# Kernel tuning notes

Hardware: AMD Instinct MI355X
Metric: run time of the kernel (lower is better)

## Reference

```python
import jax, jax.numpy as jnp
import numpy as np

N = 50000   # nodes
E = 600000  # edges
IN = 128    # in_channels
H = 128     # hidden
G = 64      # graphs in batch


def setup_inputs() -> dict:
    key = jax.random.key(0)
    ks = jax.random.split(key, 12)
    x = jax.random.normal(ks[0], (N, IN), jnp.float32)
    edge_index = jax.random.randint(ks[1], (2, E), 0, N, dtype=jnp.int64)
    batch = jnp.sort(jax.random.randint(ks[2], (N,), 0, G, dtype=jnp.int64))

    def glorot(k, i, o):
        return jax.random.normal(k, (i, o), jnp.float32) / np.float32(np.sqrt(i))

    return {
        "x": x, "edge_index": edge_index, "batch": batch,
        "W1": glorot(ks[3], IN, H), "b1": jnp.zeros((H,), jnp.float32),
        "W2": glorot(ks[4], H, H),  "b2": jnp.zeros((H,), jnp.float32),
        "W3": glorot(ks[5], H, H),  "b3": jnp.zeros((H,), jnp.float32),
        "Wl": glorot(ks[6], H, 2),  "bl": jnp.zeros((2,), jnp.float32),
    }


def gcn_conv(x, W, b, src, dst, n):
    # PyG GCNConv: linear transform, add self-loops, symmetric deg^-1/2 norm, scatter-add.
    h = x @ W                                   # [n, H]
    loop = jnp.arange(n, dtype=src.dtype)
    s = jnp.concatenate([src, loop])            # [E+n]
    d = jnp.concatenate([dst, loop])
    deg = jax.ops.segment_sum(jnp.ones_like(d, jnp.float32), d, num_segments=n)
    dinv = jax.lax.rsqrt(deg)                   # deg >= 1 thanks to self-loops
    norm = dinv[s] * dinv[d]                    # [E+n]
    out = jax.ops.segment_sum(h[s] * norm[:, None], d, num_segments=n)
    return out + b


def reference(x, edge_index, batch, W1, b1, W2, b2, W3, b3, Wl, bl):
    src, dst = edge_index[0], edge_index[1]
    h = jax.nn.relu(gcn_conv(x, W1, b1, src, dst, N))
    h = jax.nn.relu(gcn_conv(h, W2, b2, src, dst, N))
    h = jax.nn.relu(gcn_conv(h, W3, b3, src, dst, N))
    # global_mean_pool over graph ids
    cnt = jax.ops.segment_sum(jnp.ones((N,), jnp.float32), batch, num_segments=G)
    pooled = jax.ops.segment_sum(h, batch, num_segments=G) / jnp.maximum(cnt, 1.0)[:, None]
    # dropout is identity in eval mode
    return pooled @ Wl + bl                     # [G, 2]
```

## Files before the change

### kernel.cpp

```cpp
#include <hip/hip_runtime.h>


#define THREADS 256
#define ELLW 48
#define ELLS 64
#define BCAP 4096
#define EPB  4096

typedef __attribute__((ext_vector_type(8))) short short8;
typedef __attribute__((ext_vector_type(4))) float f32x4;
typedef __attribute__((ext_vector_type(2))) float floatx2;

__device__ inline void bf16_split(float f, unsigned short& hi, unsigned short& lo) {
    unsigned u = __float_as_uint(f);
    unsigned r = u + 0x7FFF + ((u >> 16) & 1);
    hi = (unsigned short)(r >> 16);
    float hf = __uint_as_float((unsigned)hi << 16);
    float lf = f - hf;
    unsigned ul = __float_as_uint(lf);
    lo = (unsigned short)((ul + 0x7FFF + ((ul >> 16) & 1)) >> 16);
}
__device__ inline unsigned pack_bf16(float a, float b) {
    unsigned ua = __float_as_uint(a);
    unsigned ub = __float_as_uint(b);
    ua += 0x7FFF + ((ua >> 16) & 1);
    ub += 0x7FFF + ((ub >> 16) & 1);
    return (ua >> 16) | (ub & 0xFFFF0000u);
}
__device__ inline floatx2 fp8x2_to_f32(unsigned short u) {
    return __builtin_amdgcn_cvt_pk_f32_fp8((int)(unsigned)u, false);
}
__device__ inline unsigned char f32_to_fp8(float v) {
    int pk = __builtin_amdgcn_cvt_pk_fp8_f32(v, v, 0, false);
    return (unsigned char)(pk & 0xFF);
}

__global__ __launch_bounds__(THREADS) void prep_k(const float* __restrict__ W1,
                                                  const float* __restrict__ W2,
                                                  const float* __restrict__ W3,
                                                  unsigned* __restrict__ wf,
                                                  const int* __restrict__ batch,
                                                  int* __restrict__ gstart,
                                                  int* __restrict__ gcur,
                                                  int n, int gtot, int nb) {
    int b = blockIdx.x;
    if (b < 3) {
        const float* W = (b == 0) ? W1 : (b == 1) ? W2 : W3;
        unsigned* o_hi = wf + (size_t)b * 16384;
        unsigned* o_lo = o_hi + 8192;
        for (int o = threadIdx.x; o < 8192; o += THREADS) {
            int d = o & 3, l = (o >> 2) & 63, ts = o >> 8;
            int s = ts & 3, t = ts >> 2;
            int k = s * 32 + ((l >> 4) << 3) + d * 2;
            int nn = t * 16 + (l & 15);
            float v0 = W[k * 128 + nn];
            float v1 = W[(k + 1) * 128 + nn];
            unsigned short h0, l0, h1, l1;
            bf16_split(v0, h0, l0);
            bf16_split(v1, h1, l1);
            o_hi[o] = (unsigned)h0 | ((unsigned)h1 << 16);
            o_lo[o] = (unsigned)l0 | ((unsigned)l1 << 16);
        }
    } else if (b == 3) {
        int t = threadIdx.x;
        if (t <= gtot) {
            int lo = 0, hi = n;
            while (lo < hi) {
                int mid = (lo + hi) >> 1;
                if (batch[mid] < t) lo = mid + 1; else hi = mid;
            }
            gstart[t] = lo;
        }
    } else {
        int t = threadIdx.x;
        if (t < nb) gcur[t] = 0;
    }
}

__global__ __launch_bounds__(THREADS) void part1_k(const int* __restrict__ src,
                                                   const int* __restrict__ dst,
                                                   int* __restrict__ gcur,
                                                   unsigned* __restrict__ region,
                                                   int e, int nb) {
    __shared__ int hist[256];
    __shared__ int base[256];
    int tid = threadIdx.x;
    hist[tid] = 0;
    __syncthreads();
    int start = blockIdx.x * EPB;
#pragma unroll
    for (int j = 0; j < EPB / THREADS; ++j) {
        int i = start + j * THREADS + tid;
        if (i < e) atomicAdd(&hist[dst[i] >> 8], 1);
    }
    __syncthreads();
    if (tid < nb) base[tid] = atomicAdd(&gcur[tid], hist[tid]);
    hist[tid] = 0;
    __syncthreads();
#pragma unroll
    for (int j = 0; j < EPB / THREADS; ++j) {
        int i = start + j * THREADS + tid;
        if (i < e) {
            int d = dst[i], s = src[i];
            int bk = d >> 8;
            int lp = atomicAdd(&hist[bk], 1);
            int pos = base[bk] + lp;
            if (pos < BCAP)
                region[(size_t)bk * BCAP + pos] = ((unsigned)(d & 255) << 16) | (unsigned)s;
        }
    }
}

__global__ __launch_bounds__(THREADS) void part2_k(const unsigned* __restrict__ region,
                                                   const int* __restrict__ gcur,
                                                   int* __restrict__ ell, int n) {
    __shared__ int cnt[256];
    int tid = threadIdx.x;
    int b = blockIdx.x;
    cnt[tid] = 0;
    __syncthreads();
    int nbk = min(gcur[b], BCAP);
    for (int i = tid; i < nbk; i += THREADS) {
        unsigned u = region[(size_t)b * BCAP + i];
        int dloc = (int)(u >> 16);
        int pos = atomicAdd(&cnt[dloc], 1);
        if (pos < ELLW)
            ell[(size_t)(b * 256 + dloc) * ELLS + 1 + pos] = (int)(u & 0xFFFFu);
    }
    __syncthreads();
    int node = b * 256 + tid;
    if (node < n) ell[(size_t)node * ELLS] = cnt[tid];
}

template <bool ABF16>
__global__ __launch_bounds__(THREADS) void mfma_gemm_k(const void* __restrict__ Av,
                                                       const unsigned* __restrict__ wf,
                                                       const int* __restrict__ ell,
                                                       unsigned char* __restrict__ g8,
                                                       int n) {
    __shared__ unsigned wls[16384];
    int tid = threadIdx.x;
    int lane = tid & 63;
    int r0 = blockIdx.x * 64 + (tid >> 6) * 16;

    for (int i = tid; i < 4096; i += THREADS)
        ((uint4*)wls)[i] = ((const uint4*)wf)[i];

    f32x4 acc[8];
#pragma unroll
    for (int t = 0; t < 8; ++t) acc[t] = (f32x4){0.f, 0.f, 0.f, 0.f};

    int arow = min(r0 + (lane & 15), n - 1);
    int kcol = (lane >> 4) << 3;

    short8 ah[4], al[4];
    if (ABF16) {
        const unsigned short* A = (const unsigned short*)Av;
#pragma unroll
        for (int s = 0; s < 4; ++s)
            ah[s] = *(const short8*)&A[(size_t)arow * 128 + kcol + s * 32];
    } else {
        const float* A = (const float*)Av;
        float4 v0[4], v1[4];
#pragma unroll
        for (int s = 0; s < 4; ++s) {
            v0[s] = *(const float4*)&A[(size_t)arow * 128 + kcol + s * 32];
            v1[s] = *(const float4*)&A[(size_t)arow * 128 + kcol + s * 32 + 4];
        }
#pragma unroll
        for (int s = 0; s < 4; ++s) {
            unsigned short h[8], lo[8];
            bf16_split(v0[s].x, h[0], lo[0]); bf16_split(v0[s].y, h[1], lo[1]);
            bf16_split(v0[s].z, h[2], lo[2]); bf16_split(v0[s].w, h[3], lo[3]);
            bf16_split(v1[s].x, h[4], lo[4]); bf16_split(v1[s].y, h[5], lo[5]);
            bf16_split(v1[s].z, h[6], lo[6]); bf16_split(v1[s].w, h[7], lo[7]);
#pragma unroll
            for (int j = 0; j < 8; ++j) { ah[s][j] = (short)h[j]; al[s][j] = (short)lo[j]; }
        }
    }

    __syncthreads();

#pragma unroll
    for (int s = 0; s < 4; ++s) {
#pragma unroll
        for (int t = 0; t < 8; ++t) {
            int base = (t * 4 + s) * 256 + lane * 4;
            short8 bh = *(short8*)&wls[base];
            short8 bl = *(short8*)&wls[8192 + base];
            acc[t] = __builtin_amdgcn_mfma_f32_16x16x32_bf16(ah[s], bh, acc[t], 0, 0, 0);
            if (!ABF16)
                acc[t] = __builtin_amdgcn_mfma_f32_16x16x32_bf16(al[s], bh, acc[t], 0, 0, 0);
            acc[t] = __builtin_amdgcn_mfma_f32_16x16x32_bf16(ah[s], bl, acc[t], 0, 0, 0);
        }
    }

    int rbase = r0 + ((lane >> 4) << 2);
#pragma unroll
    for (int reg = 0; reg < 4; ++reg) {
        int rr = rbase + reg;
        if (rr < n) {
            float dv = rsqrtf(1.f + (float)ell[(size_t)rr * ELLS]);
#pragma unroll
            for (int t = 0; t < 8; ++t)
                g8[(size_t)rr * 128 + t * 16 + (lane & 15)] = f32_to_fp8(acc[t][reg] * dv);
        }
    }
}

__global__ __launch_bounds__(THREADS) void aggregate_k(const unsigned short* __restrict__ g8u,
                                                       const int* __restrict__ ell,
                                                       const float* __restrict__ bias,
                                                       unsigned* __restrict__ h16,
                                                       int n) {
    int wave = (blockIdx.x * THREADS + threadIdx.x) >> 6;
    int lane = threadIdx.x & 63;
    if (wave >= n) return;

    int v = ell[(size_t)wave * ELLS + lane];
    int cnt_true = __shfl(v, 0);
    int deg = min(cnt_true, ELLW);

    floatx2 fs = fp8x2_to_f32(g8u[(size_t)wave * 64 + lane]);
    float ax0 = fs.x, ay0 = fs.y;
    float ax1 = 0.f, ay1 = 0.f, ax2 = 0.f, ay2 = 0.f, ax3 = 0.f, ay3 = 0.f;
    float ax4 = 0.f, ay4 = 0.f, ax5 = 0.f, ay5 = 0.f, ax6 = 0.f, ay6 = 0.f;
    float ax7 = 0.f, ay7 = 0.f;

    for (int k = 0; k < deg; k += 8) {
        int s0 = __shfl(v, k + 1);
        int s1 = __shfl(v, min(k + 2, deg));
        int s2 = __shfl(v, min(k + 3, deg));
        int s3 = __shfl(v, min(k + 4, deg));
        int s4 = __shfl(v, min(k + 5, deg));
        int s5 = __shfl(v, min(k + 6, deg));
        int s6 = __shfl(v, min(k + 7, deg));
        int s7 = __shfl(v, min(k + 8, deg));
        float m1 = (k + 1 < deg) ? 1.f : 0.f;
        float m2 = (k + 2 < deg) ? 1.f : 0.f;
        float m3 = (k + 3 < deg) ? 1.f : 0.f;
        float m4 = (k + 4 < deg) ? 1.f : 0.f;
        float m5 = (k + 5 < deg) ? 1.f : 0.f;
        float m6 = (k + 6 < deg) ? 1.f : 0.f;
        float m7 = (k + 7 < deg) ? 1.f : 0.f;
        unsigned short q0 = g8u[(size_t)s0 * 64 + lane];
        unsigned short q1 = g8u[(size_t)s1 * 64 + lane];
        unsigned short q2 = g8u[(size_t)s2 * 64 + lane];
        unsigned short q3 = g8u[(size_t)s3 * 64 + lane];
        unsigned short q4 = g8u[(size_t)s4 * 64 + lane];
        unsigned short q5 = g8u[(size_t)s5 * 64 + lane];
        unsigned short q6 = g8u[(size_t)s6 * 64 + lane];
        unsigned short q7 = g8u[(size_t)s7 * 64 + lane];
        floatx2 f0 = fp8x2_to_f32(q0);
        floatx2 f1 = fp8x2_to_f32(q1);
        floatx2 f2 = fp8x2_to_f32(q2);
        floatx2 f3 = fp8x2_to_f32(q3);
        floatx2 f4 = fp8x2_to_f32(q4);
        floatx2 f5 = fp8x2_to_f32(q5);
        floatx2 f6 = fp8x2_to_f32(q6);
        floatx2 f7 = fp8x2_to_f32(q7);
        ax0 += f0.x;                ay0 += f0.y;
        ax1 = fmaf(m1, f1.x, ax1);  ay1 = fmaf(m1, f1.y, ay1);
        ax2 = fmaf(m2, f2.x, ax2);  ay2 = fmaf(m2, f2.y, ay2);
        ax3 = fmaf(m3, f3.x, ax3);  ay3 = fmaf(m3, f3.y, ay3);
        ax4 = fmaf(m4, f4.x, ax4);  ay4 = fmaf(m4, f4.y, ay4);
        ax5 = fmaf(m5, f5.x, ax5);  ay5 = fmaf(m5, f5.y, ay5);
        ax6 = fmaf(m6, f6.x, ax6);  ay6 = fmaf(m6, f6.y, ay6);
        ax7 = fmaf(m7, f7.x, ax7);  ay7 = fmaf(m7, f7.y, ay7);
    }
    ax0 += (ax1 + ax2) + (ax3 + ax4) + (ax5 + ax6) + ax7;
    ay0 += (ay1 + ay2) + (ay3 + ay4) + (ay5 + ay6) + ay7;

    float d = rsqrtf(1.f + (float)cnt_true);
    float2 bb = ((const float2*)bias)[lane];
    float ox = fmaxf(fmaf(d, ax0, bb.x), 0.f);
    float oy = fmaxf(fmaf(d, ay0, bb.y), 0.f);
    h16[(size_t)wave * 64 + lane] = pack_bf16(ox, oy);
}

#define PSLICES 8
__global__ __launch_bounds__(THREADS) void pool_k(const unsigned* __restrict__ h16,
                                                  const int* __restrict__ gstart,
                                                  float* __restrict__ partial) {
    int gph = blockIdx.x, s = blockIdx.y;
    int start = gstart[gph], end = gstart[gph + 1];
    int len = end - start;
    int chunk = (len + PSLICES - 1) / PSLICES;
    int rs = start + s * chunk;
    int re = min(rs + chunk, end);
    int c = threadIdx.x & 63, half = threadIdx.x >> 6;
    float sx = 0.f, sy = 0.f;
    for (int r = rs + half; r < re; r += 4) {
        unsigned u = h16[(size_t)r * 64 + c];
        sx += __uint_as_float(u << 16);
        sy += __uint_as_float(u & 0xFFFF0000u);
    }
    __shared__ float shx[4][64], shy[4][64];
    shx[half][c] = sx;
    shy[half][c] = sy;
    __syncthreads();
    if (half == 0) {
        sx = shx[0][c] + shx[1][c] + shx[2][c] + shx[3][c];
        sy = shy[0][c] + shy[1][c] + shy[2][c] + shy[3][c];
        partial[(gph * PSLICES + s) * 128 + c * 2] = sx;
        partial[(gph * PSLICES + s) * 128 + c * 2 + 1] = sy;
    }
}

__global__ __launch_bounds__(128) void final_k(const float* __restrict__ partial,
                                               const int* __restrict__ gstart,
                                               const float* __restrict__ Wl,
                                               const float* __restrict__ bl,
                                               float* __restrict__ out, int gtot) {
    int t = threadIdx.x;
    int gph = t >> 1, j = t & 1;
    if (gph >= gtot) return;
    float cnt = fmaxf((float)(gstart[gph + 1] - gstart[gph]), 1.f);
    float sacc = 0.f;
    for (int k = 0; k < 128; ++k) {
        float v = 0.f;
#pragma unroll
        for (int sb = 0; sb < PSLICES; ++sb)
            v += partial[(gph * PSLICES + sb) * 128 + k];
        sacc = fmaf(v, Wl[k * 2 + j], sacc);
    }
    out[gph * 2 + j] = sacc / cnt + bl[j];
}

extern "C" void kernel_launch(void* const* d_in, const int* in_sizes, int n_in,
                              void* d_out, int out_size, void* d_ws, size_t ws_size,
                              hipStream_t stream) {
    const float* x  = (const float*)d_in[0];
    const int* ei   = (const int*)d_in[1];
    const int* batch= (const int*)d_in[2];
    const float* W1 = (const float*)d_in[3];
    const float* b1 = (const float*)d_in[4];
    const float* W2 = (const float*)d_in[5];
    const float* b2 = (const float*)d_in[6];
    const float* W3 = (const float*)d_in[7];
    const float* b3 = (const float*)d_in[8];
    const float* Wl = (const float*)d_in[9];
    const float* bl = (const float*)d_in[10];
    float* out = (float*)d_out;

    const int N = in_sizes[0] / 128;
    const int E = in_sizes[1] / 2;
    const int G = out_size / 2;
    const int* src = ei;
    const int* dst = ei + E;
    const int NB = (N + 255) >> 8;

    char* ws = (char*)d_ws;
    size_t off = 0;
    auto alloc = [&](size_t bytes) -> void* {
        void* p = ws + off;
        off = (off + bytes + 255) & ~(size_t)255;
        return p;
    };
    unsigned char* g8 = (unsigned char*)alloc((size_t)N * 128);
    unsigned* h16   = (unsigned*)alloc((size_t)N * 64 * 4);
    int* ell        = (int*)alloc((size_t)N * ELLS * 4);
    unsigned* wf    = (unsigned*)alloc((size_t)3 * 16384 * 4);
    unsigned* region= (unsigned*)alloc((size_t)NB * BCAP * 4);
    int* gcur       = (int*)alloc((size_t)NB * 4);
    float* partial  = (float*)alloc((size_t)G * PSLICES * 128 * 4);
    int* gstart     = (int*)alloc((size_t)(G + 1) * 4);
    (void)ws_size;

    int grid1 = (E + EPB - 1) / EPB;
    int gemmGrid = (N + 63) / 64;
    int aggGrid = (N + 3) / 4;
    unsigned short* g8u = (unsigned short*)g8;

    prep_k<<<5, THREADS, 0, stream>>>(W1, W2, W3, wf, batch, gstart, gcur, N, G, NB);
    part1_k<<<grid1, THREADS, 0, stream>>>(src, dst, gcur, region, E, NB);
    part2_k<<<NB, THREADS, 0, stream>>>(region, gcur, ell, N);

    mfma_gemm_k<false><<<gemmGrid, THREADS, 0, stream>>>(x, wf, ell, g8, N);
    aggregate_k<<<aggGrid, THREADS, 0, stream>>>(g8u, ell, b1, h16, N);
    mfma_gemm_k<true><<<gemmGrid, THREADS, 0, stream>>>(h16, wf + 16384, ell, g8, N);
    aggregate_k<<<aggGrid, THREADS, 0, stream>>>(g8u, ell, b2, h16, N);
    mfma_gemm_k<true><<<gemmGrid, THREADS, 0, stream>>>(h16, wf + 32768, ell, g8, N);
    aggregate_k<<<aggGrid, THREADS, 0, stream>>>(g8u, ell, b3, h16, N);

    dim3 poolGrid(G, PSLICES);
    pool_k<<<poolGrid, THREADS, 0, stream>>>(h16, gstart, partial);
    final_k<<<1, 128, 0, stream>>>(partial, gstart, Wl, bl, out, G);
}
```

Measured before the change: 174.9 us.

## Pack ELL neighbor indices as 16-bit and unroll aggregation to 16 gathers

The ELL adjacency now stores neighbor indices as 16-bit values, two per dword, with the count in the first dword. This halves the row stride to 32 ints while raising capacity to 62 neighbors. The aggregation kernel unpacks indices via shuffles and issues 16 independent gathers per iteration, with masking on loaded values, to raise memory-level parallelism. It relies on source node ids fitting in 16 bits, which fails for N=50000 beyond 65535. The base already truncated to 16 bits via the region packing.

```diff
diff --git a/kernel.cpp b/kernel.cpp
--- a/kernel.cpp
+++ b/kernel.cpp
@@ -2,8 +2,8 @@
 
 
 #define THREADS 256
-#define ELLW 48
-#define ELLS 64
+#define ELLW 62
+#define ELLD 32
 #define BCAP 4096
 #define EPB  4096
 
@@ -119,17 +119,18 @@
     int b = blockIdx.x;
     cnt[tid] = 0;
     __syncthreads();
+    unsigned short* ell16 = (unsigned short*)ell;
     int nbk = min(gcur[b], BCAP);
     for (int i = tid; i < nbk; i += THREADS) {
         unsigned u = region[(size_t)b * BCAP + i];
         int dloc = (int)(u >> 16);
         int pos = atomicAdd(&cnt[dloc], 1);
         if (pos < ELLW)
-            ell[(size_t)(b * 256 + dloc) * ELLS + 1 + pos] = (int)(u & 0xFFFFu);
+            ell16[(size_t)(b * 256 + dloc) * (ELLD * 2) + 2 + pos] = (unsigned short)(u & 0xFFFFu);
     }
     __syncthreads();
     int node = b * 256 + tid;
-    if (node < n) ell[(size_t)node * ELLS] = cnt[tid];
+    if (node < n) ell[(size_t)node * ELLD] = cnt[tid];
 }
 
 template <bool ABF16>
@@ -200,7 +201,7 @@
     for (int reg = 0; reg < 4; ++reg) {
         int rr = rbase + reg;
         if (rr < n) {
-            float dv = rsqrtf(1.f + (float)ell[(size_t)rr * ELLS]);
+            float dv = rsqrtf(1.f + (float)ell[(size_t)rr * ELLD]);
 #pragma unroll
             for (int t = 0; t < 8; ++t)
                 g8[(size_t)rr * 128 + t * 16 + (lane & 15)] = f32_to_fp8(acc[t][reg] * dv);
@@ -209,7 +210,7 @@
 }
 
 __global__ __launch_bounds__(THREADS) void aggregate_k(const unsigned short* __restrict__ g8u,
-                                                       const int* __restrict__ ell,
+                                                       const unsigned* __restrict__ ell,
                                                        const float* __restrict__ bias,
                                                        unsigned* __restrict__ h16,
                                                        int n) {
@@ -217,64 +218,45 @@
     int lane = threadIdx.x & 63;
     if (wave >= n) return;
 
-    int v = ell[(size_t)wave * ELLS + lane];
-    int cnt_true = __shfl(v, 0);
+    unsigned v = ell[(size_t)wave * ELLD + (lane & 31)];
+    int cnt_true = (int)__shfl((int)v, 0);
     int deg = min(cnt_true, ELLW);
+    int dm1 = max(deg - 1, 0);
 
     floatx2 fs = fp8x2_to_f32(g8u[(size_t)wave * 64 + lane]);
-    float ax0 = fs.x, ay0 = fs.y;
-    float ax1 = 0.f, ay1 = 0.f, ax2 = 0.f, ay2 = 0.f, ax3 = 0.f, ay3 = 0.f;
-    float ax4 = 0.f, ay4 = 0.f, ax5 = 0.f, ay5 = 0.f, ax6 = 0.f, ay6 = 0.f;
-    float ax7 = 0.f, ay7 = 0.f;
-
-    for (int k = 0; k < deg; k += 8) {
-        int s0 = __shfl(v, k + 1);
-        int s1 = __shfl(v, min(k + 2, deg));
-        int s2 = __shfl(v, min(k + 3, deg));
-        int s3 = __shfl(v, min(k + 4, deg));
-        int s4 = __shfl(v, min(k + 5, deg));
-        int s5 = __shfl(v, min(k + 6, deg));
-        int s6 = __shfl(v, min(k + 7, deg));
-        int s7 = __shfl(v, min(k + 8, deg));
-        float m1 = (k + 1 < deg) ? 1.f : 0.f;
-        float m2 = (k + 2 < deg) ? 1.f : 0.f;
-        float m3 = (k + 3 < deg) ? 1.f : 0.f;
-        float m4 = (k + 4 < deg) ? 1.f : 0.f;
-        float m5 = (k + 5 < deg) ? 1.f : 0.f;
-        float m6 = (k + 6 < deg) ? 1.f : 0.f;
-        float m7 = (k + 7 < deg) ? 1.f : 0.f;
-        unsigned short q0 = g8u[(size_t)s0 * 64 + lane];
-        unsigned short q1 = g8u[(size_t)s1 * 64 + lane];
-        unsigned short q2 = g8u[(size_t)s2 * 64 + lane];
-        unsigned short q3 = g8u[(size_t)s3 * 64 + lane];
-        unsigned short q4 = g8u[(size_t)s4 * 64 + lane];
-        unsigned short q5 = g8u[(size_t)s5 * 64 + lane];
-        unsigned short q6 = g8u[(size_t)s6 * 64 + lane];
-        unsigned short q7 = g8u[(size_t)s7 * 64 + lane];
-        floatx2 f0 = fp8x2_to_f32(q0);
-        floatx2 f1 = fp8x2_to_f32(q1);
-        floatx2 f2 = fp8x2_to_f32(q2);
-        floatx2 f3 = fp8x2_to_f32(q3);
-        floatx2 f4 = fp8x2_to_f32(q4);
-        floatx2 f5 = fp8x2_to_f32(q5);
-        floatx2 f6 = fp8x2_to_f32(q6);
-        floatx2 f7 = fp8x2_to_f32(q7);
-        ax0 += f0.x;                ay0 += f0.y;
-        ax1 = fmaf(m1, f1.x, ax1);  ay1 = fmaf(m1, f1.y, ay1);
-        ax2 = fmaf(m2, f2.x, ax2);  ay2 = fmaf(m2, f2.y, ay2);
-        ax3 = fmaf(m3, f3.x, ax3);  ay3 = fmaf(m3, f3.y, ay3);
-        ax4 = fmaf(m4, f4.x, ax4);  ay4 = fmaf(m4, f4.y, ay4);
-        ax5 = fmaf(m5, f5.x, ax5);  ay5 = fmaf(m5, f5.y, ay5);
-        ax6 = fmaf(m6, f6.x, ax6);  ay6 = fmaf(m6, f6.y, ay6);
-        ax7 = fmaf(m7, f7.x, ax7);  ay7 = fmaf(m7, f7.y, ay7);
-    }
-    ax0 += (ax1 + ax2) + (ax3 + ax4) + (ax5 + ax6) + ax7;
-    ay0 += (ay1 + ay2) + (ay3 + ay4) + (ay5 + ay6) + ay7;
+    float ax[8], ay[8];
+    ax[0] = fs.x; ay[0] = fs.y;
+#pragma unroll
+    for (int i = 1; i < 8; ++i) { ax[i] = 0.f; ay[i] = 0.f; }
+
+    for (int k = 0; k < deg; k += 16) {
+        int s[16];
+#pragma unroll
+        for (int j = 0; j < 16; ++j) {
+            int jj = min(k + j, dm1);
+            unsigned dw = (unsigned)__shfl((int)v, 1 + (jj >> 1));
+            s[j] = (int)((dw >> ((jj & 1) << 4)) & 0xFFFFu);
+        }
+        unsigned short q[16];
+#pragma unroll
+        for (int j = 0; j < 16; ++j) {
+            unsigned short t = g8u[(size_t)s[j] * 64 + lane];
+            q[j] = (k + j < deg) ? t : (unsigned short)0;
+        }
+#pragma unroll
+        for (int j = 0; j < 16; ++j) {
+            floatx2 f = fp8x2_to_f32(q[j]);
+            ax[j & 7] += f.x;
+            ay[j & 7] += f.y;
+        }
+    }
+    float sx = ((ax[0] + ax[1]) + (ax[2] + ax[3])) + ((ax[4] + ax[5]) + (ax[6] + ax[7]));
+    float sy = ((ay[0] + ay[1]) + (ay[2] + ay[3])) + ((ay[4] + ay[5]) + (ay[6] + ay[7]));
 
     float d = rsqrtf(1.f + (float)cnt_true);
     float2 bb = ((const float2*)bias)[lane];
-    float ox = fmaxf(fmaf(d, ax0, bb.x), 0.f);
-    float oy = fmaxf(fmaf(d, ay0, bb.y), 0.f);
+    float ox = fmaxf(fmaf(d, sx, bb.x), 0.f);
+    float oy = fmaxf(fmaf(d, sy, bb.y), 0.f);
     h16[(size_t)wave * 64 + lane] = pack_bf16(ox, oy);
 }
 
@@ -359,7 +341,7 @@
     };
     unsigned char* g8 = (unsigned char*)alloc((size_t)N * 128);
     unsigned* h16   = (unsigned*)alloc((size_t)N * 64 * 4);
-    int* ell        = (int*)alloc((size_t)N * ELLS * 4);
+    int* ell        = (int*)alloc((size_t)N * ELLD * 4);
     unsigned* wf    = (unsigned*)alloc((size_t)3 * 16384 * 4);
     unsigned* region= (unsigned*)alloc((size_t)NB * BCAP * 4);
     int* gcur       = (int*)alloc((size_t)NB * 4);
@@ -377,11 +359,11 @@
     part2_k<<<NB, THREADS, 0, stream>>>(region, gcur, ell, N);
 
     mfma_gemm_k<false><<<gemmGrid, THREADS, 0, stream>>>(x, wf, ell, g8, N);
-    aggregate_k<<<aggGrid, THREADS, 0, stream>>>(g8u, ell, b1, h16, N);
+    aggregate_k<<<aggGrid, THREADS, 0, stream>>>(g8u, (const unsigned*)ell, b1, h16, N);
     mfma_gemm_k<true><<<gemmGrid, THREADS, 0, stream>>>(h16, wf + 16384, ell, g8, N);
-    aggregate_k<<<aggGrid, THREADS, 0, stream>>>(g8u, ell, b2, h16, N);
+    aggregate_k<<<aggGrid, THREADS, 0, stream>>>(g8u, (const unsigned*)ell, b2, h16, N);
     mfma_gemm_k<true><<<gemmGrid, THREADS, 0, stream>>>(h16, wf + 32768, ell, g8, N);
-    aggregate_k<<<aggGrid, THREADS, 0, stream>>>(g8u, ell, b3, h16, N);
+    aggregate_k<<<aggGrid, THREADS, 0, stream>>>(g8u, (const unsigned*)ell, b3, h16, N);
 
     dim3 poolGrid(G, PSLICES);
     pool_k<<<poolGrid, THREADS, 0, stream>>>(h16, gstart, partial);
```

After: 196.1 us. 12.1% more time.
